# Optimization experiments

Measured on AMD Instinct MI355X. Metric: run time of the kernel, lower is better.

The kernel has to match this reference:

```python
import jax, jax.numpy as jnp
import numpy as np

NMAX = 1
MARGIN = 0.2
N, D = 16384, 256

def setup_inputs() -> dict:
    key = jax.random.key(0)
    k1, k2 = jax.random.split(key)
    imgs = jax.random.normal(k1, (N, D), dtype=jnp.float32)
    caps = jax.random.normal(k2, (N, D), dtype=jnp.float32)
    return {"imgs": imgs, "caps": caps}

def reference(imgs, caps):
    # scores[i, j] = <img_i, cap_j>
    scores = imgs @ caps.T                      # [N, N]
    diag = jnp.diagonal(scores)                 # [N]
    s = scores - 2.0 * jnp.diag(diag)
    # hardest negatives per caption (top over image axis = rows) -> [nmax, N]
    max_c = jax.lax.top_k(s.T, NMAX)[0].T
    # hardest negatives per image (top over caption axis = cols) -> [N, nmax]
    max_i = jax.lax.top_k(s, NMAX)[0]
    neg_cap = jnp.sum(jnp.maximum(max_c + (MARGIN - diag)[None, :], 0.0))
    neg_img = jnp.sum(jnp.maximum(max_i + (MARGIN - diag)[:, None], 0.0))
    return neg_cap + neg_img
```

## Files before the change

kernel.cpp:

```cpp
#include <hip/hip_runtime.h>
#include <hip/hip_bf16.h>
#include <hip/hip_fp8.h>
#include <stdint.h>
#include <math.h>

#define NN 16384
#define DD 256
#define MARGIN_F 0.2f

typedef __attribute__((ext_vector_type(8))) int int32x8;
typedef __attribute__((ext_vector_type(4))) float f32x4;

__device__ inline unsigned fkey(float f) {
    unsigned b = __float_as_uint(f);
    return (b & 0x80000000u) ? ~b : (b | 0x80000000u);
}
__device__ inline float fdec(unsigned k) {
    return __uint_as_float((k & 0x80000000u) ? (k ^ 0x80000000u) : ~k);
}
#define NEG_INF_KEY 0x007FFFFFu

__device__ inline void gload16(const void* g, void* l) {
    __builtin_amdgcn_global_load_lds(
        (const __attribute__((address_space(1))) void*)g,
        (__attribute__((address_space(3))) void*)l, 16, 0, 0);
}

__device__ inline unsigned pk8(float4 v) {
    __hip_fp8_e4m3 q0(v.x), q1(v.y), q2(v.z), q3(v.w);
    return (unsigned)q0.__x | ((unsigned)q1.__x << 8) |
           ((unsigned)q2.__x << 16) | ((unsigned)q3.__x << 24);
}

__global__ __launch_bounds__(256) void fused_prep_kernel(
    const float* __restrict__ imgs, const float* __restrict__ caps,
    unsigned char* __restrict__ imgs8, unsigned char* __restrict__ caps8,
    float* __restrict__ diag, unsigned* __restrict__ rowmax,
    unsigned* __restrict__ colmax) {
    const int i = (blockIdx.x << 2) + (threadIdx.x >> 6);
    const int l = threadIdx.x & 63;
    const float4* a4 = reinterpret_cast<const float4*>(imgs + (size_t)i * DD);
    const float4* b4 = reinterpret_cast<const float4*>(caps + (size_t)i * DD);
    float4 av = a4[l];
    float4 bv = b4[l];
    reinterpret_cast<unsigned*>(imgs8 + (size_t)i * DD)[l] = pk8(av);
    reinterpret_cast<unsigned*>(caps8 + (size_t)i * DD)[l] = pk8(bv);
    float s = av.x * bv.x + av.y * bv.y + av.z * bv.z + av.w * bv.w;
    #pragma unroll
    for (int off = 32; off > 0; off >>= 1) s += __shfl_down(s, off);
    if (l == 0) {
        diag[i] = s;
        rowmax[i] = NEG_INF_KEY;
        colmax[i] = NEG_INF_KEY;
    }
}

__global__ __launch_bounds__(256, 2) void score_max_kernel(
    const unsigned char* __restrict__ imgs8,
    const unsigned char* __restrict__ caps8,
    const float* __restrict__ diag,
    unsigned* __restrict__ rowmax, unsigned* __restrict__ colmax) {

    __shared__ char lds[49152];
    float* clds = reinterpret_cast<float*>(lds + 32768);

    const int bid   = blockIdx.x;
    const int panel = bid >> 2;
    const int strip = bid & 3;
    const int brow  = panel << 7;
    const int scol  = strip << 12;

    const int t    = threadIdx.x;
    const int wid  = t >> 6;
    const int lane = t & 63;
    const int rg   = lane >> 4;
    const int cl   = lane & 15;

    #pragma unroll
    for (int i = 0; i < 16; ++i) clds[t + (i << 8)] = -INFINITY;

    {
        const int sl = t & 15;
        const int rw = t >> 4;
        const int srcoff = (((sl >> 1) ^ (rw & 7)) << 5) + ((sl & 1) << 4);
        const unsigned char* src =
            imgs8 + (((size_t)(brow + rw)) << 8) + srcoff;
        #pragma unroll
        for (int i = 0; i < 8; ++i)
            gload16(src + ((size_t)i << 12), lds + t * 16 + i * 4096);
    }
    __syncthreads();

    int32x8 af[8][2];
    #pragma unroll
    for (int m = 0; m < 8; ++m) {
        const int row = m * 16 + cl;
        #pragma unroll
        for (int ks = 0; ks < 2; ++ks)
            af[m][ks] = *reinterpret_cast<const int32x8*>(
                lds + row * 256 + (((rg + (ks << 2)) ^ (cl & 7)) << 5));
    }

    float rmx[8][4];
    #pragma unroll
    for (int m = 0; m < 8; ++m)
        #pragma unroll
        for (int r = 0; r < 4; ++r) rmx[m][r] = -INFINITY;

    const unsigned char* pb =
        caps8 + (((size_t)(scol + (wid << 4) + cl)) << 8) + (rg << 5);

    const f32x4 zv = (f32x4){0.f, 0.f, 0.f, 0.f};
    #define SCL 0x7F7F7F7F

    int32x8 b0 = *reinterpret_cast<const int32x8*>(pb);
    int32x8 b1 = *reinterpret_cast<const int32x8*>(pb + 128);

    for (int h = 0; h < 64; ++h) {
        const int cb = scol + (h << 6);
        const int hn = (h < 63) ? h + 1 : h;
        const unsigned char* pn = pb + ((size_t)hn << 14);

        int32x8 bn0 = *reinterpret_cast<const int32x8*>(pn);
        int32x8 bn1 = *reinterpret_cast<const int32x8*>(pn + 128);

        f32x4 acc[8];
        __builtin_amdgcn_s_setprio(1);
        #pragma unroll
        for (int m = 0; m < 8; ++m)
            acc[m] = __builtin_amdgcn_mfma_scale_f32_16x16x128_f8f6f4(
                af[m][0], b0, zv, 0, 0, 0, SCL, 0, SCL);
        #pragma unroll
        for (int m = 0; m < 8; ++m)
            acc[m] = __builtin_amdgcn_mfma_scale_f32_16x16x128_f8f6f4(
                af[m][1], b1, acc[m], 0, 0, 0, SCL, 0, SCL);
        __builtin_amdgcn_s_setprio(0);

        const int cfb = cb + (wid << 4);
        if (cfb < brow + 128 && cfb + 16 > brow) {
            #pragma unroll
            for (int m = 0; m < 8; ++m)
                #pragma unroll
                for (int r = 0; r < 4; ++r) {
                    const int gi = brow + m * 16 + (rg << 2) + r;
                    if (gi - cfb == cl) acc[m][r] = -diag[gi];
                }
        }

        #pragma unroll
        for (int m = 0; m < 8; ++m)
            #pragma unroll
            for (int r = 0; r < 4; ++r)
                rmx[m][r] = fmaxf(rmx[m][r], acc[m][r]);

        {
            float v = fmaxf(fmaxf(acc[0][0], acc[0][1]),
                            fmaxf(acc[0][2], acc[0][3]));
            #pragma unroll
            for (int m = 1; m < 8; ++m)
                v = fmaxf(v, fmaxf(fmaxf(acc[m][0], acc[m][1]),
                                   fmaxf(acc[m][2], acc[m][3])));
            v = fmaxf(v, __shfl_xor(v, 16));
            v = fmaxf(v, __shfl_xor(v, 32));
            if (rg == 0) {
                const int c = cfb + cl - scol;
                clds[c] = fmaxf(clds[c], v);
            }
        }

        b0 = bn0;
        b1 = bn1;
    }

    #pragma unroll
    for (int m = 0; m < 8; ++m)
        #pragma unroll
        for (int r = 0; r < 4; ++r) {
            float v = rmx[m][r];
            v = fmaxf(v, __shfl_xor(v, 1));
            v = fmaxf(v, __shfl_xor(v, 2));
            v = fmaxf(v, __shfl_xor(v, 4));
            v = fmaxf(v, __shfl_xor(v, 8));
            if (cl == 0)
                atomicMax(&rowmax[brow + m * 16 + (rg << 2) + r], fkey(v));
        }

    __syncthreads();
    #pragma unroll
    for (int i = 0; i < 16; ++i) {
        const int c = t + (i << 8);
        atomicMax(&colmax[scol + c], fkey(clds[c]));
    }
}

__global__ __launch_bounds__(1024) void finalize_kernel(
    const float* __restrict__ diag,
    const unsigned* __restrict__ rowmax,
    const unsigned* __restrict__ colmax,
    float* __restrict__ out) {
    __shared__ float red[1024];
    int t = threadIdx.x;
    float s = 0.f;
    for (int idx = t; idx < 2 * NN; idx += 1024) {
        int i = idx & (NN - 1);
        float mx = fdec((idx < NN) ? colmax[i] : rowmax[i]);
        s += fmaxf(mx + (MARGIN_F - diag[i]), 0.f);
    }
    red[t] = s;
    __syncthreads();
    for (int off = 512; off > 0; off >>= 1) {
        if (t < off) red[t] += red[t + off];
        __syncthreads();
    }
    if (t == 0) out[0] = red[0];
}

extern "C" void kernel_launch(void* const* d_in, const int* in_sizes, int n_in,
                              void* d_out, int out_size, void* d_ws, size_t ws_size,
                              hipStream_t stream) {
    const float* imgs = reinterpret_cast<const float*>(d_in[0]);
    const float* caps = reinterpret_cast<const float*>(d_in[1]);

    float* diag          = reinterpret_cast<float*>(d_ws);
    unsigned* rowmax     = reinterpret_cast<unsigned*>(diag + NN);
    unsigned* colmax     = rowmax + NN;
    unsigned char* imgs8 = reinterpret_cast<unsigned char*>(colmax + NN);
    unsigned char* caps8 = imgs8 + (size_t)NN * DD;

    fused_prep_kernel<<<NN / 4, 256, 0, stream>>>(imgs, caps, imgs8, caps8,
                                                  diag, rowmax, colmax);

    score_max_kernel<<<512, 256, 0, stream>>>(imgs8, caps8, diag,
                                              rowmax, colmax);

    finalize_kernel<<<1, 1024, 0, stream>>>(diag, rowmax, colmax,
                                            reinterpret_cast<float*>(d_out));
}
```

Before: 95.16 us.

## Double-buffer MFMA accumulators to overlap epilogue with next chunk's MFMAs

```diff
diff --git a/kernel.cpp b/kernel.cpp
--- a/kernel.cpp
+++ b/kernel.cpp
@@ -113,64 +113,77 @@
     const f32x4 zv = (f32x4){0.f, 0.f, 0.f, 0.f};
     #define SCL 0x7F7F7F7F
 
-    int32x8 b0 = *reinterpret_cast<const int32x8*>(pb);
-    int32x8 b1 = *reinterpret_cast<const int32x8*>(pb + 128);
-
-    for (int h = 0; h < 64; ++h) {
-        const int cb = scol + (h << 6);
-        const int hn = (h < 63) ? h + 1 : h;
-        const unsigned char* pn = pb + ((size_t)hn << 14);
-
-        int32x8 bn0 = *reinterpret_cast<const int32x8*>(pn);
-        int32x8 bn1 = *reinterpret_cast<const int32x8*>(pn + 128);
-
-        f32x4 acc[8];
-        __builtin_amdgcn_s_setprio(1);
-        #pragma unroll
-        for (int m = 0; m < 8; ++m)
-            acc[m] = __builtin_amdgcn_mfma_scale_f32_16x16x128_f8f6f4(
-                af[m][0], b0, zv, 0, 0, 0, SCL, 0, SCL);
-        #pragma unroll
-        for (int m = 0; m < 8; ++m)
-            acc[m] = __builtin_amdgcn_mfma_scale_f32_16x16x128_f8f6f4(
-                af[m][1], b1, acc[m], 0, 0, 0, SCL, 0, SCL);
-        __builtin_amdgcn_s_setprio(0);
-
-        const int cfb = cb + (wid << 4);
-        if (cfb < brow + 128 && cfb + 16 > brow) {
-            #pragma unroll
-            for (int m = 0; m < 8; ++m)
-                #pragma unroll
-                for (int r = 0; r < 4; ++r) {
-                    const int gi = brow + m * 16 + (rg << 2) + r;
-                    if (gi - cfb == cl) acc[m][r] = -diag[gi];
-                }
-        }
-
-        #pragma unroll
-        for (int m = 0; m < 8; ++m)
-            #pragma unroll
-            for (int r = 0; r < 4; ++r)
-                rmx[m][r] = fmaxf(rmx[m][r], acc[m][r]);
-
-        {
-            float v = fmaxf(fmaxf(acc[0][0], acc[0][1]),
-                            fmaxf(acc[0][2], acc[0][3]));
-            #pragma unroll
-            for (int m = 1; m < 8; ++m)
-                v = fmaxf(v, fmaxf(fmaxf(acc[m][0], acc[m][1]),
-                                   fmaxf(acc[m][2], acc[m][3])));
-            v = fmaxf(v, __shfl_xor(v, 16));
-            v = fmaxf(v, __shfl_xor(v, 32));
-            if (rg == 0) {
-                const int c = cfb + cl - scol;
-                clds[c] = fmaxf(clds[c], v);
-            }
-        }
-
-        b0 = bn0;
-        b1 = bn1;
-    }
+    f32x4 accA[8], accB[8];
+
+    #define MFMA_CHUNK(ACC, B0, B1) {                                          \
+        __builtin_amdgcn_s_setprio(1);                                         \
+        _Pragma("unroll")                                                      \
+        for (int m = 0; m < 8; ++m)                                            \
+            ACC[m] = __builtin_amdgcn_mfma_scale_f32_16x16x128_f8f6f4(         \
+                af[m][0], B0, zv, 0, 0, 0, SCL, 0, SCL);                       \
+        _Pragma("unroll")                                                      \
+        for (int m = 0; m < 8; ++m)                                            \
+            ACC[m] = __builtin_amdgcn_mfma_scale_f32_16x16x128_f8f6f4(         \
+                af[m][1], B1, ACC[m], 0, 0, 0, SCL, 0, SCL);                   \
+        __builtin_amdgcn_s_setprio(0);                                         \
+    }
+
+    #define EPI(ACC, CB) {                                                     \
+        const int cfb_ = (CB) + (wid << 4);                                    \
+        if (cfb_ < brow + 128 && cfb_ + 16 > brow) {                           \
+            _Pragma("unroll")                                                  \
+            for (int m = 0; m < 8; ++m)                                        \
+                _Pragma("unroll")                                              \
+                for (int r = 0; r < 4; ++r) {                                  \
+                    const int gi_ = brow + m * 16 + (rg << 2) + r;             \
+                    if (gi_ - cfb_ == cl) ACC[m][r] = -diag[gi_];              \
+                }                                                              \
+        }                                                                      \
+        _Pragma("unroll")                                                      \
+        for (int m = 0; m < 8; ++m)                                            \
+            _Pragma("unroll")                                                  \
+            for (int r = 0; r < 4; ++r)                                        \
+                rmx[m][r] = fmaxf(rmx[m][r], ACC[m][r]);                       \
+        {                                                                      \
+            float v_ = fmaxf(ACC[0][0], ACC[0][1]);                            \
+            v_ = fmaxf(fmaxf(v_, ACC[0][2]), ACC[0][3]);                       \
+            _Pragma("unroll")                                                  \
+            for (int m = 1; m < 8; ++m) {                                      \
+                v_ = fmaxf(fmaxf(v_, ACC[m][0]), ACC[m][1]);                   \
+                v_ = fmaxf(fmaxf(v_, ACC[m][2]), ACC[m][3]);                   \
+            }                                                                  \
+            v_ = fmaxf(v_, __shfl_xor(v_, 16));                                \
+            v_ = fmaxf(v_, __shfl_xor(v_, 32));                                \
+            if (rg == 0) {                                                     \
+                const int c_ = cfb_ + cl - scol;                               \
+                clds[c_] = fmaxf(clds[c_], v_);                                \
+            }                                                                  \
+        }                                                                      \
+    }
+
+    int32x8 bA0 = *reinterpret_cast<const int32x8*>(pb);
+    int32x8 bA1 = *reinterpret_cast<const int32x8*>(pb + 128);
+
+    for (int h = 0; h < 64; h += 2) {
+        const unsigned char* p1 = pb + ((size_t)(h + 1) << 14);
+        int32x8 bB0 = *reinterpret_cast<const int32x8*>(p1);
+        int32x8 bB1 = *reinterpret_cast<const int32x8*>(p1 + 128);
+
+        MFMA_CHUNK(accA, bA0, bA1);
+        if (h > 0) EPI(accB, scol + ((h - 1) << 6));
+
+        const int h2 = (h + 2 < 64) ? h + 2 : h;
+        const unsigned char* p2 = pb + ((size_t)h2 << 14);
+        bA0 = *reinterpret_cast<const int32x8*>(p2);
+        bA1 = *reinterpret_cast<const int32x8*>(p2 + 128);
+
+        MFMA_CHUNK(accB, bB0, bB1);
+        EPI(accA, scol + (h << 6));
+    }
+    EPI(accB, scol + (63 << 6));
+
+    #undef MFMA_CHUNK
+    #undef EPI
 
     #pragma unroll
     for (int m = 0; m < 8; ++m)
```

Measured after the change: 305.5 us. 221% more time.
